# Kernel tuning notes

Hardware: AMD Instinct MI355X
Metric: run time of the kernel (lower is better)

## Reference

```python
import jax, jax.numpy as jnp
import numpy as np

C, N, E = 256, 256, 2048          # subgraphs, nodes/subgraph, edges/subgraph
F_IN, NHID, DDI = 128, 128, 256
K1, K2, K3 = 128, 64, 32          # top-k sizes for pooling_ratio=0.5
P, B = 16, 16                     # DAG hierarchy: P parents x B leaf children
GN = C + P + 1                    # global DAG nodes (leaves + parents + root)
GE = 8192                         # global pos/neg edge count


def setup_inputs():
    key = jax.random.key(0)
    ks = jax.random.split(key, 16)
    inp = {
        "x": jax.random.normal(ks[0], (C, N, F_IN), jnp.float32),
        "edge_index": jax.random.randint(ks[1], (C, 2, E), 0, N),
        "edge_weight": jax.random.uniform(ks[2], (C, E), dtype=jnp.float32),
        "global_edge_index": jax.random.randint(ks[3], (2, GE), 0, GN),
        "neg_edge_index": jax.random.randint(ks[4], (2, GE), 0, GN),
    }
    names = [("W1", F_IN, NHID), ("Wp1", NHID, 1), ("W2", NHID, NHID),
             ("Wp2", NHID, 1), ("W3", NHID, NHID), ("Wp3", NHID, 1),
             ("Wg", 6 * NHID, DDI), ("Wl1", DDI, DDI), ("Wl2", DDI, DDI)]
    for i, (nm, fi, fo) in enumerate(names):
        inp[nm] = jax.random.normal(ks[5 + i], (fi, fo), jnp.float32) / np.sqrt(fi)
        inp["b" + nm[1:]] = jnp.zeros((fo,), jnp.float32)
    return inp


def gcn(x, ei, ew, W, b):
    """PyG GCNConv with self-loops: D^-1/2 (A+I) D^-1/2 X W + b."""
    n = x.shape[0]
    h = x @ W
    row, col = ei[0], ei[1]
    deg = 1.0 + jax.ops.segment_sum(ew, col, num_segments=n)
    dis = jax.lax.rsqrt(deg)
    norm = dis[row] * ew * dis[col]                       # [E]
    agg = jax.ops.segment_sum(norm[:, None] * h[row], col, num_segments=n)
    return agg + h / deg[:, None] + b


def sag_pool(x, ei, ew, Ws, bs, k):
    """SAGPooling: GCN score, per-graph top-k, gate by tanh(score), edge filter."""
    n = x.shape[0]
    score = gcn(x, ei, ew, Ws, bs)[:, 0]
    vals, perm = jax.lax.top_k(score, k)
    x_new = x[perm] * jnp.tanh(vals)[:, None]
    newid = jnp.full((n,), -1, jnp.int32).at[perm].set(jnp.arange(k, dtype=jnp.int32))
    r, c = newid[ei[0]], newid[ei[1]]
    keep = (r >= 0) & (c >= 0)
    ei_new = jnp.where(keep, jnp.stack([r, c]), 0)        # dropped edges -> node 0
    ew_new = jnp.where(keep, ew, 0.0)                     # with zero weight
    return x_new, ei_new, ew_new


def _subgraph(x, ei, ew, W1, b1, Wp1, bp1, W2, b2, Wp2, bp2, W3, b3, Wp3, bp3):
    x = jax.nn.relu(gcn(x, ei, ew, W1, b1))
    x, ei, ew = sag_pool(x, ei, ew, Wp1, bp1, K1)
    x1 = jnp.concatenate([x.max(0), x.mean(0)])           # gmp||gap, batch all-zero
    x = jax.nn.relu(gcn(x, ei, ew, W2, b2))
    x, ei, ew = sag_pool(x, ei, ew, Wp2, bp2, K2)
    x2 = jnp.concatenate([x.max(0), x.mean(0)])
    x = jax.nn.relu(gcn(x, ei, ew, W3, b3))
    x, ei, ew = sag_pool(x, ei, ew, Wp3, bp3, K3)
    x3 = jnp.concatenate([x.max(0), x.mean(0)])
    return jnp.concatenate([x1, x2, x3])                  # [6*NHID]


def reference(x, edge_index, edge_weight, global_edge_index, neg_edge_index,
              W1, b1, Wp1, bp1, W2, b2, Wp2, bp2, W3, b3, Wp3, bp3,
              Wg, bg, Wl1, bl1, Wl2, bl2):
    # per-class subgraph pipeline, vmapped over the C subgraphs
    leaf = jax.vmap(_subgraph, in_axes=(0, 0, 0) + (None,) * 12)(
        x, edge_index, edge_weight,
        W1, b1, Wp1, bp1, W2, b2, Wp2, bp2, W3, b3, Wp3, bp3)   # [C, 6*NHID]
    # Get_Fs: mean-aggregate children features up the DAG (fixed 2-level + root)
    parent = leaf.reshape(P, B, -1).mean(axis=1)                # [P, 6*NHID]
    root = parent.mean(axis=0, keepdims=True)                   # [1, 6*NHID]
    gfeat = jnp.concatenate([leaf, parent, root], axis=0)       # [GN, 6*NHID]
    # global GCN (unit edge weights)
    gx = jax.nn.relu(gcn(gfeat, global_edge_index,
                         jnp.ones((GE,), gfeat.dtype), Wg, bg)) # [GN, DDI]
    class_embedding = gx[:C]
    # feature_split + lin1/lin2 + dot-product scores
    pos_s = gx[global_edge_index[0]] @ Wl1 + bl1
    pos_t = gx[global_edge_index[1]] @ Wl2 + bl2
    neg_s = gx[neg_edge_index[0]] @ Wl1 + bl1
    neg_t = gx[neg_edge_index[1]] @ Wl2 + bl2
    pos = jnp.sum(pos_s * pos_t, axis=1)
    neg = jnp.sum(neg_s * neg_t, axis=1)
    # BCEWithLogits: targets 1 for pos, 0 for neg
    loss = jnp.mean(jax.nn.softplus(-pos)) + jnp.mean(jax.nn.softplus(neg))
    return class_embedding, loss
```

## Files before the change

kernel.cpp:

```cpp
#include <hip/hip_runtime.h>
#include <math.h>

#define NT 1024
#define EDGES 2048
#define SENT 0xFFFF

struct SmemA {
  float xbuf[256 * 128];
  unsigned short rc[EDGES];
  float ewl[EDGES];
  unsigned short csr_row[EDGES];
  float csr_coef[EDGES];
  float degs[256];
  float diss[256];
  int   csr_off[257];
  int   csr_cnt[256];
  float hsv[256];
  float scorev[256];
  float vals[128];
  short perm[128];
  signed char newid[256];
};

__device__ __forceinline__ float4* xvec(float* xb, int row, int c4) {
  return reinterpret_cast<float4*>(xb + (row << 7) + ((c4 ^ (row & 7)) << 2));
}
__device__ __forceinline__ int xidx(int row, int col) {
  return (row << 7) + ((((col >> 2) ^ (row & 7)) << 2) | (col & 3));
}

template<int NN, int K, bool FIRST, bool REMAP>
__device__ __forceinline__ void run_stage(
    SmemA& sm,
    const float* __restrict__ xg,
    const int* __restrict__ eic,
    const float* __restrict__ ewc,
    const float* __restrict__ W,
    const float* __restrict__ b,
    const float* __restrict__ Wp,
    const float* __restrict__ bp,
    float* __restrict__ leaf_out,
    float& lmax, float& lmean)
{
  constexpr int NPT  = NN / 64;
  constexpr int Q    = NN / 64;
  constexpr int SEG  = NT / NN;
  constexpr int LEN  = NN / SEG;
  constexpr int LOG  = (NN == 256) ? 8 : (NN == 128 ? 7 : 6);
  const int tid  = threadIdx.x;
  const int lane = tid & 63;
  const int fbase = __builtin_amdgcn_readfirstlane((tid >> 6) << 3);
  const int c4b   = fbase >> 2;

  if (FIRST) {
    if (tid < NN) { sm.degs[tid] = 1.0f; sm.csr_cnt[tid] = 0; }
    __syncthreads();
    const float4* xg4 = reinterpret_cast<const float4*>(xg);
    for (int i = tid; i < 256 * 32; i += NT) {
      const float4 v = xg4[i];
      *xvec(sm.xbuf, i >> 5, i & 31) = v;
    }
    for (int e = tid; e < EDGES; e += NT) {
      const int row = eic[e], col = eic[EDGES + e];
      const float w = ewc[e];
      sm.rc[e]  = (unsigned short)((row << 8) | col);
      sm.ewl[e] = w;
      atomicAdd(&sm.degs[col], w);
      atomicAdd(&sm.csr_cnt[col], 1);
    }
    __syncthreads();
  }

  if (tid < NN) sm.diss[tid] = rsqrtf(sm.degs[tid]);
  if (tid < 64) {
    int c[Q], pre[Q];
    int tot = 0;
#pragma unroll
    for (int i = 0; i < Q; i++) { c[i] = sm.csr_cnt[tid * Q + i]; pre[i] = tot; tot += c[i]; }
    int inc = tot;
#pragma unroll
    for (int d = 1; d < 64; d <<= 1) {
      const int o = __shfl_up(inc, d, 64);
      if (tid >= d) inc += o;
    }
    const int base = inc - tot;
    if (tid == 0) sm.csr_off[0] = 0;
#pragma unroll
    for (int i = 0; i < Q; i++) {
      sm.csr_off[tid * Q + i + 1] = base + pre[i] + c[i];
      sm.csr_cnt[tid * Q + i] = 0;
    }
  }
  __syncthreads();

  for (int e = tid; e < EDGES; e += NT) {
    const unsigned short r = sm.rc[e];
    if (FIRST || r != SENT) {
      const int row = r >> 8, col = r & 255;
      const int p = atomicAdd(&sm.csr_cnt[col], 1);
      const int s = sm.csr_off[col] + p;
      sm.csr_row[s]  = (unsigned short)row;
      sm.csr_coef[s] = sm.diss[row] * sm.ewl[e];
    }
  }
  __syncthreads();

  float acc[NPT][8];
#pragma unroll
  for (int i = 0; i < NPT; i++)
#pragma unroll
    for (int j = 0; j < 8; j++) acc[i][j] = 0.0f;

#pragma unroll 4
  for (int k4 = 0; k4 < 32; k4++) {
    float4 xv[NPT];
#pragma unroll
    for (int i = 0; i < NPT; i++) xv[i] = *xvec(sm.xbuf, lane + (i << 6), k4);
#pragma unroll
    for (int kk = 0; kk < 4; kk++) {
      const float* wr = W + (((k4 << 2) + kk) << 7) + fbase;
      const float4 wa = *reinterpret_cast<const float4*>(wr);
      const float4 wb = *reinterpret_cast<const float4*>(wr + 4);
      const float wv[8] = {wa.x, wa.y, wa.z, wa.w, wb.x, wb.y, wb.z, wb.w};
#pragma unroll
      for (int i = 0; i < NPT; i++) {
        const float xs = (kk == 0) ? xv[i].x : (kk == 1) ? xv[i].y : (kk == 2) ? xv[i].z : xv[i].w;
#pragma unroll
        for (int j = 0; j < 8; j++) acc[i][j] = fmaf(xs, wv[j], acc[i][j]);
      }
    }
  }
  __syncthreads();

#pragma unroll
  for (int i = 0; i < NPT; i++) {
    const int v = lane + (i << 6);
    *xvec(sm.xbuf, v, c4b)     = make_float4(acc[i][0], acc[i][1], acc[i][2], acc[i][3]);
    *xvec(sm.xbuf, v, c4b + 1) = make_float4(acc[i][4], acc[i][5], acc[i][6], acc[i][7]);
  }
  __syncthreads();

  float agg[NPT][8];
#pragma unroll
  for (int i = 0; i < NPT; i++) {
    const int v = lane + (i << 6);
    const int beg = sm.csr_off[v], end = sm.csr_off[v + 1];
#pragma unroll
    for (int j = 0; j < 8; j++) agg[i][j] = 0.0f;
    int r_nxt = 0; float c_nxt = 0.0f;
    if (beg < end) { r_nxt = sm.csr_row[beg]; c_nxt = sm.csr_coef[beg]; }
    for (int s = beg; s < end; ++s) {
      const int r = r_nxt; const float cf = c_nxt;
      if (s + 1 < end) { r_nxt = sm.csr_row[s + 1]; c_nxt = sm.csr_coef[s + 1]; }
      const float4 lo = *xvec(sm.xbuf, r, c4b);
      const float4 hi = *xvec(sm.xbuf, r, c4b + 1);
      agg[i][0] = fmaf(cf, lo.x, agg[i][0]);
      agg[i][1] = fmaf(cf, lo.y, agg[i][1]);
      agg[i][2] = fmaf(cf, lo.z, agg[i][2]);
      agg[i][3] = fmaf(cf, lo.w, agg[i][3]);
      agg[i][4] = fmaf(cf, hi.x, agg[i][4]);
      agg[i][5] = fmaf(cf, hi.y, agg[i][5]);
      agg[i][6] = fmaf(cf, hi.z, agg[i][6]);
      agg[i][7] = fmaf(cf, hi.w, agg[i][7]);
    }
  }
  if (tid < NN) sm.hsv[tid] = 0.0f;
  __syncthreads();

  {
    const float4 ba = *reinterpret_cast<const float4*>(b + fbase);
    const float4 bb = *reinterpret_cast<const float4*>(b + fbase + 4);
    const float bv[8] = {ba.x, ba.y, ba.z, ba.w, bb.x, bb.y, bb.z, bb.w};
#pragma unroll
    for (int i = 0; i < NPT; i++) {
      const int v = lane + (i << 6);
      const float dv = sm.diss[v];
      const float invd = 1.0f / sm.degs[v];
#pragma unroll
      for (int j = 0; j < 8; j++)
        acc[i][j] = fmaxf(fmaf(agg[i][j], dv, fmaf(acc[i][j], invd, bv[j])), 0.0f);
      *xvec(sm.xbuf, v, c4b)     = make_float4(acc[i][0], acc[i][1], acc[i][2], acc[i][3]);
      *xvec(sm.xbuf, v, c4b + 1) = make_float4(acc[i][4], acc[i][5], acc[i][6], acc[i][7]);
    }
    const float4 wa = *reinterpret_cast<const float4*>(Wp + fbase);
    const float4 wb = *reinterpret_cast<const float4*>(Wp + fbase + 4);
    const float wv[8] = {wa.x, wa.y, wa.z, wa.w, wb.x, wb.y, wb.z, wb.w};
#pragma unroll
    for (int i = 0; i < NPT; i++) {
      float part = 0.0f;
#pragma unroll
      for (int j = 0; j < 8; j++) part = fmaf(acc[i][j], wv[j], part);
      atomicAdd(&sm.hsv[lane + (i << 6)], part);
    }
  }
  __syncthreads();

  if (tid < NN) {
    const int v = tid;
    const int beg = sm.csr_off[v], end = sm.csr_off[v + 1];
    float s = 0.0f;
    for (int e2 = beg; e2 < end; e2++)
      s = fmaf(sm.csr_coef[e2], sm.hsv[sm.csr_row[e2]], s);
    sm.scorev[v] = s * sm.diss[v] + sm.hsv[v] / sm.degs[v] + bp[0];
    sm.csr_cnt[v] = 0;
  }
  __syncthreads();

  {
    const int node = tid & (NN - 1);
    const int seg  = tid >> LOG;
    const float sv = sm.scorev[node];
    int part = 0;
    const int u0 = seg * LEN;
#pragma unroll 4
    for (int u = u0; u < u0 + LEN; u++) {
      const float su = sm.scorev[u];
      part += (su > sv) || (su == sv && u < node);
    }
    if (part) atomicAdd(&sm.csr_cnt[node], part);
  }
  __syncthreads();
  if (tid < NN) {
    const int rank = sm.csr_cnt[tid];
    if (rank < K) { sm.perm[rank] = (short)tid; sm.vals[rank] = sm.scorev[tid]; sm.newid[tid] = (signed char)rank; }
    else sm.newid[tid] = -1;
    if (tid < K) { sm.degs[tid] = 1.0f; sm.csr_cnt[tid] = 0; }
  }
  __syncthreads();

  {
    constexpr int TPR = NT / K;
    constexpr int C4  = 32 / TPR;
    const int drow = tid / TPR;
    const int cc   = (tid % TPR) * C4;
    const int src  = sm.perm[drow];
    const float g  = tanhf(sm.vals[drow]);
    float4 tmp[C4];
#pragma unroll
    for (int j = 0; j < C4; j++) tmp[j] = *xvec(sm.xbuf, src, cc + j);
    __syncthreads();
#pragma unroll
    for (int j = 0; j < C4; j++) {
      tmp[j].x *= g; tmp[j].y *= g; tmp[j].z *= g; tmp[j].w *= g;
      *xvec(sm.xbuf, drow, cc + j) = tmp[j];
    }
  }
  __syncthreads();

  if (tid < 128) {
    float mx = -INFINITY, sv = 0.0f;
    for (int i = 0; i < K; i++) {
      const float v = sm.xbuf[xidx(i, tid)];
      mx = fmaxf(mx, v); sv += v;
    }
    lmax = mx;
    lmean = sv * (1.0f / K);
    leaf_out[tid] = mx;
    leaf_out[128 + tid] = lmean;
  }
  if (REMAP) {
    for (int e = tid; e < EDGES; e += NT) {
      const unsigned short r = sm.rc[e];
      if (FIRST || r != SENT) {
        const int r2 = sm.newid[r >> 8];
        const int c2 = sm.newid[r & 255];
        if (r2 < 0 || c2 < 0) sm.rc[e] = SENT;
        else {
          sm.rc[e] = (unsigned short)((r2 << 8) | c2);
          atomicAdd(&sm.degs[c2], sm.ewl[e]);
          atomicAdd(&sm.csr_cnt[c2], 1);
        }
      }
    }
  }
  __syncthreads();
}

__global__ __launch_bounds__(NT)
void stageA_kernel(const float* __restrict__ x0,
                   const int* __restrict__ ei, const float* __restrict__ ew,
                   const float* __restrict__ W1, const float* __restrict__ b1,
                   const float* __restrict__ Wp1, const float* __restrict__ bp1,
                   const float* __restrict__ W2, const float* __restrict__ b2,
                   const float* __restrict__ Wp2, const float* __restrict__ bp2,
                   const float* __restrict__ W3, const float* __restrict__ b3,
                   const float* __restrict__ Wp3, const float* __restrict__ bp3,
                   const float* __restrict__ Wg,
                   float* __restrict__ gfeat, float* __restrict__ hG)
{
  __shared__ SmemA sm;
  const int c = blockIdx.x;
  const int tid = threadIdx.x;
  if (c == 0 && tid < 256) hG[(size_t)272 * 256 + tid] = 0.0f;
  const int* eic = ei + (size_t)c * 2 * EDGES;
  const float* ewc = ew + (size_t)c * EDGES;
  const float* xgc = x0 + (size_t)c * 256 * 128;
  float* leaf = gfeat + (size_t)c * 768;
  float l0 = 0.f, l1 = 0.f, l2 = 0.f, l3 = 0.f, l4 = 0.f, l5 = 0.f;
  run_stage<256, 128, true,  true >(sm, xgc, eic, ewc, W1, b1, Wp1, bp1, leaf + 0,   l0, l1);
  run_stage<128,  64, false, true >(sm, nullptr, nullptr, nullptr, W2, b2, Wp2, bp2, leaf + 256, l2, l3);
  run_stage< 64,  32, false, false>(sm, nullptr, nullptr, nullptr, W3, b3, Wp3, bp3, leaf + 512, l4, l5);

  float* leafbuf = sm.csr_coef;
  float* hGacc   = sm.degs;
  if (tid < 256) {
    if (tid < 128) {
      leafbuf[tid]       = l0; leafbuf[128 + tid] = l1;
      leafbuf[256 + tid] = l2; leafbuf[384 + tid] = l3;
      leafbuf[512 + tid] = l4; leafbuf[640 + tid] = l5;
    }
    hGacc[tid] = 0.0f;
  }
  __syncthreads();
  {
    const int f = tid & 255, q = tid >> 8;
    const float* wgq = Wg + (size_t)(q * 192) * 256 + f;
    const float* lb  = leafbuf + q * 192;
    float p0 = 0.f, p1 = 0.f, p2 = 0.f, p3 = 0.f;
    for (int i = 0; i < 192; i += 4) {
      p0 = fmaf(lb[i],     wgq[(size_t)i * 256],      p0);
      p1 = fmaf(lb[i + 1], wgq[(size_t)(i + 1) * 256], p1);
      p2 = fmaf(lb[i + 2], wgq[(size_t)(i + 2) * 256], p2);
      p3 = fmaf(lb[i + 3], wgq[(size_t)(i + 3) * 256], p3);
    }
    atomicAdd(&hGacc[f], (p0 + p1) + (p2 + p3));
  }
  __syncthreads();
  if (tid < 256) hG[(size_t)c * 256 + tid] = hGacc[tid];
}

__global__ __launch_bounds__(NT)
void prep_k(const float* __restrict__ gfeat, const float* __restrict__ Wg,
            float* __restrict__ hG, const int* __restrict__ gei,
            float* __restrict__ degG, float* __restrict__ lacc,
            int* __restrict__ lctr) {
  const int tid = threadIdx.x;
  if (blockIdx.x == 16) {
    __shared__ int cnt[273];
    for (int i = tid; i < 273; i += NT) cnt[i] = 0;
    __syncthreads();
    for (int e = tid; e < 8192; e += NT) atomicAdd(&cnt[gei[8192 + e]], 1);
    __syncthreads();
    for (int i = tid; i < 273; i += NT) degG[i] = 1.0f + (float)cnt[i];
    if (tid == 0) { *lacc = 0.0f; *lctr = 0; }
    return;
  }
  const int p = blockIdx.x;
  __shared__ float prow[768];
  __shared__ float hGacc[256];
  for (int k = tid; k < 768; k += NT) {
    float s0 = 0.f, s1 = 0.f;
#pragma unroll
    for (int b2 = 0; b2 < 16; b2 += 2) {
      s0 += gfeat[(size_t)(p * 16 + b2) * 768 + k];
      s1 += gfeat[(size_t)(p * 16 + b2 + 1) * 768 + k];
    }
    prow[k] = (s0 + s1) * (1.0f / 16.0f);
  }
  if (tid < 256) hGacc[tid] = 0.0f;
  __syncthreads();
  {
    const int f = tid & 255, q = tid >> 8;
    const float* wgq = Wg + (size_t)(q * 192) * 256 + f;
    const float* lb  = prow + q * 192;
    float p0 = 0.f, p1 = 0.f, p2 = 0.f, p3 = 0.f;
    for (int i = 0; i < 192; i += 4) {
      p0 = fmaf(lb[i],     wgq[(size_t)i * 256],      p0);
      p1 = fmaf(lb[i + 1], wgq[(size_t)(i + 1) * 256], p1);
      p2 = fmaf(lb[i + 2], wgq[(size_t)(i + 2) * 256], p2);
      p3 = fmaf(lb[i + 3], wgq[(size_t)(i + 3) * 256], p3);
    }
    atomicAdd(&hGacc[f], (p0 + p1) + (p2 + p3));
  }
  __syncthreads();
  if (tid < 256) {
    const float hv = hGacc[tid];
    hG[(size_t)(256 + p) * 256 + tid] = hv;
    atomicAdd(&hG[(size_t)272 * 256 + tid], hv * (1.0f / 16.0f));
  }
}

__global__ __launch_bounds__(256)
void gaggemb_k(const float* __restrict__ hG, const float* __restrict__ degG,
               const int* __restrict__ gei, const float* __restrict__ bg,
               const float* __restrict__ Wl1, const float* __restrict__ bl1,
               const float* __restrict__ Wl2, const float* __restrict__ bl2,
               float* __restrict__ out_ce, float* __restrict__ A,
               float* __restrict__ B) {
  __shared__ int   lrows[512];
  __shared__ float lcoef[512];
  __shared__ float gxr[256];
  __shared__ int   lcnt;
  const int v = blockIdx.x, tid = threadIdx.x;
  if (tid == 0) lcnt = 0;
  __syncthreads();
  for (int e = tid; e < 8192; e += 256)
    if (gei[8192 + e] == v) {
      const int p = atomicAdd(&lcnt, 1);
      if (p < 512) lrows[p] = gei[e];
    }
  __syncthreads();
  const int n = min(lcnt, 512);
  for (int i = tid; i < n; i += 256) lcoef[i] = rsqrtf(degG[lrows[i]]);
  __syncthreads();
  float a0 = 0.f, a1 = 0.f, a2 = 0.f, a3 = 0.f;
  int i = 0;
  for (; i + 4 <= n; i += 4) {
    a0 = fmaf(lcoef[i],     hG[(size_t)lrows[i]     * 256 + tid], a0);
    a1 = fmaf(lcoef[i + 1], hG[(size_t)lrows[i + 1] * 256 + tid], a1);
    a2 = fmaf(lcoef[i + 2], hG[(size_t)lrows[i + 2] * 256 + tid], a2);
    a3 = fmaf(lcoef[i + 3], hG[(size_t)lrows[i + 3] * 256 + tid], a3);
  }
  for (; i < n; i++) a0 = fmaf(lcoef[i], hG[(size_t)lrows[i] * 256 + tid], a0);
  const float dg = degG[v];
  float val = ((a0 + a1) + (a2 + a3)) * rsqrtf(dg)
            + hG[(size_t)v * 256 + tid] / dg + bg[tid];
  val = fmaxf(val, 0.0f);
  gxr[tid] = val;
  if (v < 256) out_ce[(size_t)v * 256 + tid] = val;
  __syncthreads();
  float aa0 = bl1[tid], aa1 = 0.f, aa2 = 0.f, aa3 = 0.f;
  float bb0 = bl2[tid], bb1 = 0.f, bb2 = 0.f, bb3 = 0.f;
  for (int k = 0; k < 256; k += 4) {
    const float g0 = gxr[k], g1 = gxr[k + 1], g2 = gxr[k + 2], g3 = gxr[k + 3];
    aa0 = fmaf(g0, Wl1[(size_t)k * 256 + tid],       aa0);
    aa1 = fmaf(g1, Wl1[(size_t)(k + 1) * 256 + tid], aa1);
    aa2 = fmaf(g2, Wl1[(size_t)(k + 2) * 256 + tid], aa2);
    aa3 = fmaf(g3, Wl1[(size_t)(k + 3) * 256 + tid], aa3);
    bb0 = fmaf(g0, Wl2[(size_t)k * 256 + tid],       bb0);
    bb1 = fmaf(g1, Wl2[(size_t)(k + 1) * 256 + tid], bb1);
    bb2 = fmaf(g2, Wl2[(size_t)(k + 2) * 256 + tid], bb2);
    bb3 = fmaf(g3, Wl2[(size_t)(k + 3) * 256 + tid], bb3);
  }
  A[(size_t)v * 256 + tid] = (aa0 + aa1) + (aa2 + aa3);
  B[(size_t)v * 256 + tid] = (bb0 + bb1) + (bb2 + bb3);
}

__global__ __launch_bounds__(256)
void loss_k(const float* __restrict__ A, const float* __restrict__ B,
            const int* __restrict__ gei, const int* __restrict__ nei,
            float* __restrict__ acc, int* __restrict__ lctr,
            float* __restrict__ out) {
  const int gw = (blockIdx.x * blockDim.x + threadIdx.x) >> 6;
  const int lane = threadIdx.x & 63;
  float lsum = 0.0f;
  for (int idx = gw; idx < 16384; idx += 512) {
    const bool ispos = idx < 8192;
    const int e = ispos ? idx : idx - 8192;
    const int* ia = ispos ? gei : nei;
    const int s = ia[e], t = ia[8192 + e];
    float p = 0.0f;
#pragma unroll
    for (int j = 0; j < 4; j++)
      p += A[(size_t)s * 256 + lane + 64 * j] * B[(size_t)t * 256 + lane + 64 * j];
#pragma unroll
    for (int off = 32; off; off >>= 1) p += __shfl_xor(p, off, 64);
    const float z = ispos ? -p : p;
    lsum += fmaxf(z, 0.0f) + log1pf(expf(-fabsf(z)));
  }
  if (lane == 0) atomicAdd(acc, lsum);
  __syncthreads();
  if (threadIdx.x == 0) {
    __threadfence();
    const int old = atomicAdd(lctr, 1);
    if (old == (int)gridDim.x - 1) {
      const float tot = atomicAdd(acc, 0.0f);
      out[65536] = tot * (1.0f / 8192.0f);
    }
  }
}

extern "C" void kernel_launch(void* const* d_in, const int* in_sizes, int n_in,
                              void* d_out, int out_size, void* d_ws, size_t ws_size,
                              hipStream_t stream) {
  const float* x   = (const float*)d_in[0];
  const int*   ei  = (const int*)d_in[1];
  const float* ew  = (const float*)d_in[2];
  const int*   gei = (const int*)d_in[3];
  const int*   nei = (const int*)d_in[4];
  const float* W1  = (const float*)d_in[5];
  const float* b1  = (const float*)d_in[6];
  const float* Wp1 = (const float*)d_in[7];
  const float* bp1 = (const float*)d_in[8];
  const float* W2  = (const float*)d_in[9];
  const float* b2  = (const float*)d_in[10];
  const float* Wp2 = (const float*)d_in[11];
  const float* bp2 = (const float*)d_in[12];
  const float* W3  = (const float*)d_in[13];
  const float* b3  = (const float*)d_in[14];
  const float* Wp3 = (const float*)d_in[15];
  const float* bp3 = (const float*)d_in[16];
  const float* Wg  = (const float*)d_in[17];
  const float* bg  = (const float*)d_in[18];
  const float* Wl1 = (const float*)d_in[19];
  const float* bl1 = (const float*)d_in[20];
  const float* Wl2 = (const float*)d_in[21];
  const float* bl2 = (const float*)d_in[22];

  float* ws    = (float*)d_ws;
  float* gfeat = ws;
  float* hG    = gfeat + 256 * 768;
  float* degG  = hG + 273 * 256;
  float* Aemb  = degG + 288;
  float* Bemb  = Aemb + 273 * 256;
  float* lacc  = Bemb + 273 * 256;
  int*   lctr  = (int*)(lacc + 1);
  float* out   = (float*)d_out;

  stageA_kernel<<<256, NT, 0, stream>>>(x, ei, ew, W1, b1, Wp1, bp1,
                                        W2, b2, Wp2, bp2, W3, b3, Wp3, bp3,
                                        Wg, gfeat, hG);
  prep_k<<<17, NT, 0, stream>>>(gfeat, Wg, hG, gei, degG, lacc, lctr);
  gaggemb_k<<<273, 256, 0, stream>>>(hG, degG, gei, bg, Wl1, bl1, Wl2, bl2,
                                     out, Aemb, Bemb);
  loss_k<<<128, 256, 0, stream>>>(Aemb, Bemb, gei, nei, lacc, lctr, out);
}
```

Baseline: 182.5 us.

## Build global CSR once in prep kernel and fuse GCN aggregation with score projection

The global-graph aggregation kernel no longer scans all 8192 edges per destination node. The prep block now builds a CSR (offsets, source rows, rsqrt coefficients) once, and the aggregation/embedding kernel runs with 1024 threads, splitting the neighbour sum and the Wl1/Wl2 matvecs into four partial sums reduced in shared memory. In stageA, the neighbour aggregation is fused into the epilogue and score-projection loop, which removes the agg register array and one barrier, and the score loop prefetches its next edge. The trade-offs are extra global CSR writes and reads, more shared-memory partial reductions, and atomic-order nondeterminism in CSR slot assignment.

Result: no change. 185.8 us (+1.8%).

```diff
diff --git a/kernel.cpp b/kernel.cpp
--- a/kernel.cpp
+++ b/kernel.cpp
@@ -93,6 +93,7 @@
   }
   __syncthreads();
 
+  if (tid < NN) sm.hsv[tid] = 0.0f;
   for (int e = tid; e < EDGES; e += NT) {
     const unsigned short r = sm.rc[e];
     if (FIRST || r != SENT) {
@@ -140,67 +141,70 @@
   }
   __syncthreads();
 
-  float agg[NPT][8];
-#pragma unroll
-  for (int i = 0; i < NPT; i++) {
-    const int v = lane + (i << 6);
-    const int beg = sm.csr_off[v], end = sm.csr_off[v + 1];
-#pragma unroll
-    for (int j = 0; j < 8; j++) agg[i][j] = 0.0f;
-    int r_nxt = 0; float c_nxt = 0.0f;
-    if (beg < end) { r_nxt = sm.csr_row[beg]; c_nxt = sm.csr_coef[beg]; }
-    for (int s = beg; s < end; ++s) {
-      const int r = r_nxt; const float cf = c_nxt;
-      if (s + 1 < end) { r_nxt = sm.csr_row[s + 1]; c_nxt = sm.csr_coef[s + 1]; }
-      const float4 lo = *xvec(sm.xbuf, r, c4b);
-      const float4 hi = *xvec(sm.xbuf, r, c4b + 1);
-      agg[i][0] = fmaf(cf, lo.x, agg[i][0]);
-      agg[i][1] = fmaf(cf, lo.y, agg[i][1]);
-      agg[i][2] = fmaf(cf, lo.z, agg[i][2]);
-      agg[i][3] = fmaf(cf, lo.w, agg[i][3]);
-      agg[i][4] = fmaf(cf, hi.x, agg[i][4]);
-      agg[i][5] = fmaf(cf, hi.y, agg[i][5]);
-      agg[i][6] = fmaf(cf, hi.z, agg[i][6]);
-      agg[i][7] = fmaf(cf, hi.w, agg[i][7]);
-    }
-  }
-  if (tid < NN) sm.hsv[tid] = 0.0f;
-  __syncthreads();
-
   {
     const float4 ba = *reinterpret_cast<const float4*>(b + fbase);
     const float4 bb = *reinterpret_cast<const float4*>(b + fbase + 4);
     const float bv[8] = {ba.x, ba.y, ba.z, ba.w, bb.x, bb.y, bb.z, bb.w};
-#pragma unroll
-    for (int i = 0; i < NPT; i++) {
-      const int v = lane + (i << 6);
-      const float dv = sm.diss[v];
-      const float invd = 1.0f / sm.degs[v];
-#pragma unroll
-      for (int j = 0; j < 8; j++)
-        acc[i][j] = fmaxf(fmaf(agg[i][j], dv, fmaf(acc[i][j], invd, bv[j])), 0.0f);
-      *xvec(sm.xbuf, v, c4b)     = make_float4(acc[i][0], acc[i][1], acc[i][2], acc[i][3]);
-      *xvec(sm.xbuf, v, c4b + 1) = make_float4(acc[i][4], acc[i][5], acc[i][6], acc[i][7]);
-    }
     const float4 wa = *reinterpret_cast<const float4*>(Wp + fbase);
     const float4 wb = *reinterpret_cast<const float4*>(Wp + fbase + 4);
     const float wv[8] = {wa.x, wa.y, wa.z, wa.w, wb.x, wb.y, wb.z, wb.w};
 #pragma unroll
     for (int i = 0; i < NPT; i++) {
+      const int v = lane + (i << 6);
+      const int beg = sm.csr_off[v], end = sm.csr_off[v + 1];
+      float ag[8] = {0.f, 0.f, 0.f, 0.f, 0.f, 0.f, 0.f, 0.f};
+      float4 plo = make_float4(0.f, 0.f, 0.f, 0.f), phi = plo;
+      float cf_nxt = 0.0f;
+      if (beg < end) {
+        const int r0 = sm.csr_row[beg];
+        cf_nxt = sm.csr_coef[beg];
+        plo = *xvec(sm.xbuf, r0, c4b);
+        phi = *xvec(sm.xbuf, r0, c4b + 1);
+      }
+      for (int s = beg; s < end; ++s) {
+        const float4 lo = plo, hi = phi;
+        const float cf = cf_nxt;
+        if (s + 1 < end) {
+          const int rn = sm.csr_row[s + 1];
+          cf_nxt = sm.csr_coef[s + 1];
+          plo = *xvec(sm.xbuf, rn, c4b);
+          phi = *xvec(sm.xbuf, rn, c4b + 1);
+        }
+        ag[0] = fmaf(cf, lo.x, ag[0]); ag[1] = fmaf(cf, lo.y, ag[1]);
+        ag[2] = fmaf(cf, lo.z, ag[2]); ag[3] = fmaf(cf, lo.w, ag[3]);
+        ag[4] = fmaf(cf, hi.x, ag[4]); ag[5] = fmaf(cf, hi.y, ag[5]);
+        ag[6] = fmaf(cf, hi.z, ag[6]); ag[7] = fmaf(cf, hi.w, ag[7]);
+      }
+      const float dv = sm.diss[v];
+      const float invd = 1.0f / sm.degs[v];
       float part = 0.0f;
 #pragma unroll
-      for (int j = 0; j < 8; j++) part = fmaf(acc[i][j], wv[j], part);
-      atomicAdd(&sm.hsv[lane + (i << 6)], part);
-    }
-  }
-  __syncthreads();
-
+      for (int j = 0; j < 8; j++) {
+        acc[i][j] = fmaxf(fmaf(ag[j], dv, fmaf(acc[i][j], invd, bv[j])), 0.0f);
+        part = fmaf(acc[i][j], wv[j], part);
+      }
+      atomicAdd(&sm.hsv[v], part);
+    }
+  }
+  __syncthreads();
+
+#pragma unroll
+  for (int i = 0; i < NPT; i++) {
+    const int v = lane + (i << 6);
+    *xvec(sm.xbuf, v, c4b)     = make_float4(acc[i][0], acc[i][1], acc[i][2], acc[i][3]);
+    *xvec(sm.xbuf, v, c4b + 1) = make_float4(acc[i][4], acc[i][5], acc[i][6], acc[i][7]);
+  }
   if (tid < NN) {
     const int v = tid;
     const int beg = sm.csr_off[v], end = sm.csr_off[v + 1];
     float s = 0.0f;
-    for (int e2 = beg; e2 < end; e2++)
-      s = fmaf(sm.csr_coef[e2], sm.hsv[sm.csr_row[e2]], s);
+    int r_nxt = 0; float c_nxt = 0.0f;
+    if (beg < end) { r_nxt = sm.csr_row[beg]; c_nxt = sm.csr_coef[beg]; }
+    for (int e2 = beg; e2 < end; e2++) {
+      const int r = r_nxt; const float cf = c_nxt;
+      if (e2 + 1 < end) { r_nxt = sm.csr_row[e2 + 1]; c_nxt = sm.csr_coef[e2 + 1]; }
+      s = fmaf(cf, sm.hsv[r], s);
+    }
     sm.scorev[v] = s * sm.diss[v] + sm.hsv[v] / sm.degs[v] + bp[0];
     sm.csr_cnt[v] = 0;
   }
@@ -318,7 +322,7 @@
     const float* lb  = leafbuf + q * 192;
     float p0 = 0.f, p1 = 0.f, p2 = 0.f, p3 = 0.f;
     for (int i = 0; i < 192; i += 4) {
-      p0 = fmaf(lb[i],     wgq[(size_t)i * 256],      p0);
+      p0 = fmaf(lb[i],     wgq[(size_t)i * 256],       p0);
       p1 = fmaf(lb[i + 1], wgq[(size_t)(i + 1) * 256], p1);
       p2 = fmaf(lb[i + 2], wgq[(size_t)(i + 2) * 256], p2);
       p3 = fmaf(lb[i + 3], wgq[(size_t)(i + 3) * 256], p3);
@@ -332,16 +336,45 @@
 __global__ __launch_bounds__(NT)
 void prep_k(const float* __restrict__ gfeat, const float* __restrict__ Wg,
             float* __restrict__ hG, const int* __restrict__ gei,
-            float* __restrict__ degG, float* __restrict__ lacc,
-            int* __restrict__ lctr) {
+            float* __restrict__ degG, int* __restrict__ goff,
+            int* __restrict__ gcsr_row, float* __restrict__ gcsr_coef,
+            float* __restrict__ lacc, int* __restrict__ lctr) {
   const int tid = threadIdx.x;
   if (blockIdx.x == 16) {
-    __shared__ int cnt[273];
-    for (int i = tid; i < 273; i += NT) cnt[i] = 0;
+    __shared__ int cnt[320];
+    __shared__ int off[321];
+    __shared__ int fc[288];
+    for (int i = tid; i < 320; i += NT) cnt[i] = 0;
+    if (tid < 288) fc[tid] = 0;
     __syncthreads();
     for (int e = tid; e < 8192; e += NT) atomicAdd(&cnt[gei[8192 + e]], 1);
     __syncthreads();
-    for (int i = tid; i < 273; i += NT) degG[i] = 1.0f + (float)cnt[i];
+    if (tid < 64) {
+      int c[5], pre[5];
+      int tot = 0;
+#pragma unroll
+      for (int i = 0; i < 5; i++) { c[i] = cnt[tid * 5 + i]; pre[i] = tot; tot += c[i]; }
+      int inc = tot;
+#pragma unroll
+      for (int d = 1; d < 64; d <<= 1) {
+        const int o = __shfl_up(inc, d, 64);
+        if (tid >= d) inc += o;
+      }
+      const int base = inc - tot;
+      if (tid == 0) off[0] = 0;
+#pragma unroll
+      for (int i = 0; i < 5; i++) off[tid * 5 + i + 1] = base + pre[i] + c[i];
+    }
+    if (tid < 273) degG[tid] = 1.0f + (float)cnt[tid];
+    __syncthreads();
+    for (int e = tid; e < 8192; e += NT) {
+      const int col = gei[8192 + e], row = gei[e];
+      const int p = atomicAdd(&fc[col], 1);
+      const int s = off[col] + p;
+      gcsr_row[s]  = row;
+      gcsr_coef[s] = rsqrtf(1.0f + (float)cnt[row]);
+    }
+    if (tid < 274) goff[tid] = off[tid];
     if (tid == 0) { *lacc = 0.0f; *lctr = 0; }
     return;
   }
@@ -365,7 +398,7 @@
     const float* lb  = prow + q * 192;
     float p0 = 0.f, p1 = 0.f, p2 = 0.f, p3 = 0.f;
     for (int i = 0; i < 192; i += 4) {
-      p0 = fmaf(lb[i],     wgq[(size_t)i * 256],      p0);
+      p0 = fmaf(lb[i],     wgq[(size_t)i * 256],       p0);
       p1 = fmaf(lb[i + 1], wgq[(size_t)(i + 1) * 256], p1);
       p2 = fmaf(lb[i + 2], wgq[(size_t)(i + 2) * 256], p2);
       p3 = fmaf(lb[i + 3], wgq[(size_t)(i + 3) * 256], p3);
@@ -380,60 +413,49 @@
   }
 }
 
-__global__ __launch_bounds__(256)
+__global__ __launch_bounds__(NT)
 void gaggemb_k(const float* __restrict__ hG, const float* __restrict__ degG,
-               const int* __restrict__ gei, const float* __restrict__ bg,
+               const int* __restrict__ goff, const int* __restrict__ gcsr_row,
+               const float* __restrict__ gcsr_coef, const float* __restrict__ bg,
                const float* __restrict__ Wl1, const float* __restrict__ bl1,
                const float* __restrict__ Wl2, const float* __restrict__ bl2,
                float* __restrict__ out_ce, float* __restrict__ A,
                float* __restrict__ B) {
-  __shared__ int   lrows[512];
-  __shared__ float lcoef[512];
+  __shared__ float pacc[1024];
+  __shared__ float pacc2[1024];
   __shared__ float gxr[256];
-  __shared__ int   lcnt;
   const int v = blockIdx.x, tid = threadIdx.x;
-  if (tid == 0) lcnt = 0;
-  __syncthreads();
-  for (int e = tid; e < 8192; e += 256)
-    if (gei[8192 + e] == v) {
-      const int p = atomicAdd(&lcnt, 1);
-      if (p < 512) lrows[p] = gei[e];
-    }
-  __syncthreads();
-  const int n = min(lcnt, 512);
-  for (int i = tid; i < n; i += 256) lcoef[i] = rsqrtf(degG[lrows[i]]);
-  __syncthreads();
-  float a0 = 0.f, a1 = 0.f, a2 = 0.f, a3 = 0.f;
-  int i = 0;
-  for (; i + 4 <= n; i += 4) {
-    a0 = fmaf(lcoef[i],     hG[(size_t)lrows[i]     * 256 + tid], a0);
-    a1 = fmaf(lcoef[i + 1], hG[(size_t)lrows[i + 1] * 256 + tid], a1);
-    a2 = fmaf(lcoef[i + 2], hG[(size_t)lrows[i + 2] * 256 + tid], a2);
-    a3 = fmaf(lcoef[i + 3], hG[(size_t)lrows[i + 3] * 256 + tid], a3);
-  }
-  for (; i < n; i++) a0 = fmaf(lcoef[i], hG[(size_t)lrows[i] * 256 + tid], a0);
-  const float dg = degG[v];
-  float val = ((a0 + a1) + (a2 + a3)) * rsqrtf(dg)
-            + hG[(size_t)v * 256 + tid] / dg + bg[tid];
-  val = fmaxf(val, 0.0f);
-  gxr[tid] = val;
-  if (v < 256) out_ce[(size_t)v * 256 + tid] = val;
-  __syncthreads();
-  float aa0 = bl1[tid], aa1 = 0.f, aa2 = 0.f, aa3 = 0.f;
-  float bb0 = bl2[tid], bb1 = 0.f, bb2 = 0.f, bb3 = 0.f;
-  for (int k = 0; k < 256; k += 4) {
-    const float g0 = gxr[k], g1 = gxr[k + 1], g2 = gxr[k + 2], g3 = gxr[k + 3];
-    aa0 = fmaf(g0, Wl1[(size_t)k * 256 + tid],       aa0);
-    aa1 = fmaf(g1, Wl1[(size_t)(k + 1) * 256 + tid], aa1);
-    aa2 = fmaf(g2, Wl1[(size_t)(k + 2) * 256 + tid], aa2);
-    aa3 = fmaf(g3, Wl1[(size_t)(k + 3) * 256 + tid], aa3);
-    bb0 = fmaf(g0, Wl2[(size_t)k * 256 + tid],       bb0);
-    bb1 = fmaf(g1, Wl2[(size_t)(k + 1) * 256 + tid], bb1);
-    bb2 = fmaf(g2, Wl2[(size_t)(k + 2) * 256 + tid], bb2);
-    bb3 = fmaf(g3, Wl2[(size_t)(k + 3) * 256 + tid], bb3);
-  }
-  A[(size_t)v * 256 + tid] = (aa0 + aa1) + (aa2 + aa3);
-  B[(size_t)v * 256 + tid] = (bb0 + bb1) + (bb2 + bb3);
+  const int f = tid & 255, q = tid >> 8;
+  const int beg = goff[v], end = goff[v + 1];
+  float s = 0.f;
+  for (int i = beg + q; i < end; i += 4)
+    s = fmaf(gcsr_coef[i], hG[(size_t)gcsr_row[i] * 256 + f], s);
+  pacc[tid] = s;
+  __syncthreads();
+  if (tid < 256) {
+    const float dg = degG[v];
+    float val = (pacc[tid] + pacc[256 + tid] + pacc[512 + tid] + pacc[768 + tid]) * rsqrtf(dg)
+              + hG[(size_t)v * 256 + tid] / dg + bg[tid];
+    val = fmaxf(val, 0.0f);
+    gxr[tid] = val;
+    if (v < 256) out_ce[(size_t)v * 256 + tid] = val;
+  }
+  __syncthreads();
+  {
+    const int k0 = q << 6;
+    float a = 0.f, b2 = 0.f;
+    for (int k = k0; k < k0 + 64; k++) {
+      const float g = gxr[k];
+      a  = fmaf(g, Wl1[(size_t)k * 256 + f], a);
+      b2 = fmaf(g, Wl2[(size_t)k * 256 + f], b2);
+    }
+    pacc[tid] = a; pacc2[tid] = b2;
+  }
+  __syncthreads();
+  if (tid < 256) {
+    A[(size_t)v * 256 + tid] = pacc[tid] + pacc[256 + tid] + pacc[512 + tid] + pacc[768 + tid] + bl1[tid];
+    B[(size_t)v * 256 + tid] = pacc2[tid] + pacc2[256 + tid] + pacc2[512 + tid] + pacc2[768 + tid] + bl2[tid];
+  }
 }
 
 __global__ __launch_bounds__(256)
@@ -497,21 +519,25 @@
   const float* Wl2 = (const float*)d_in[21];
   const float* bl2 = (const float*)d_in[22];
 
-  float* ws    = (float*)d_ws;
-  float* gfeat = ws;
-  float* hG    = gfeat + 256 * 768;
-  float* degG  = hG + 273 * 256;
-  float* Aemb  = degG + 288;
-  float* Bemb  = Aemb + 273 * 256;
-  float* lacc  = Bemb + 273 * 256;
-  int*   lctr  = (int*)(lacc + 1);
-  float* out   = (float*)d_out;
+  float* ws       = (float*)d_ws;
+  float* gfeat    = ws;
+  float* hG       = gfeat + 256 * 768;
+  float* degG     = hG + 273 * 256;
+  float* Aemb     = degG + 288;
+  float* Bemb     = Aemb + 273 * 256;
+  float* lacc     = Bemb + 273 * 256;
+  int*   lctr     = (int*)(lacc + 1);
+  int*   goff     = lctr + 1;
+  int*   gcsr_row = goff + 288;
+  float* gcsr_coef= (float*)(gcsr_row + 8192);
+  float* out      = (float*)d_out;
 
   stageA_kernel<<<256, NT, 0, stream>>>(x, ei, ew, W1, b1, Wp1, bp1,
                                         W2, b2, Wp2, bp2, W3, b3, Wp3, bp3,
                                         Wg, gfeat, hG);
-  prep_k<<<17, NT, 0, stream>>>(gfeat, Wg, hG, gei, degG, lacc, lctr);
-  gaggemb_k<<<273, 256, 0, stream>>>(hG, degG, gei, bg, Wl1, bl1, Wl2, bl2,
-                                     out, Aemb, Bemb);
+  prep_k<<<17, NT, 0, stream>>>(gfeat, Wg, hG, gei, degG, goff,
+                                gcsr_row, gcsr_coef, lacc, lctr);
+  gaggemb_k<<<273, NT, 0, stream>>>(hG, degG, goff, gcsr_row, gcsr_coef, bg,
+                                    Wl1, bl1, Wl2, bl2, out, Aemb, Bemb);
   loss_k<<<128, 256, 0, stream>>>(Aemb, Bemb, gei, nei, lacc, lctr, out);
 }
```
